# Performance work log

Hardware: AMD Instinct MI355X
Metric: run time of the kernel (lower is better)

The kernel has to match this reference:

```python
import jax, jax.numpy as jnp
import numpy as np

N = 100000   # nodes
E = 600000   # edges
D_IN, D_H, D_OUT = 128, 128, 128


def glorot(key, shape):
    lim = float(np.sqrt(6.0 / (shape[0] + shape[1])))
    return jax.random.uniform(key, shape, jnp.float32, -lim, lim)


def setup_inputs() -> dict:
    key = jax.random.key(0)
    k1, k2, k3, k4 = jax.random.split(key, 4)
    x = jax.random.normal(k1, (N, D_IN), jnp.float32)
    edge_index = jax.random.randint(k2, (2, E), 0, N, jnp.int64)
    W1 = glorot(k3, (D_IN, D_H))
    b1 = jnp.zeros((D_H,), jnp.float32)
    W2 = glorot(k4, (D_H, D_OUT))
    b2 = jnp.zeros((D_OUT,), jnp.float32)
    return {"x": x, "W1": W1, "b1": b1, "W2": W2, "b2": b2, "edge_index": edge_index}


def gcn_conv(x, W, b, src, dst, n):
    # GCNConv: D^{-1/2}(A+I)D^{-1/2} X W + b  (self loops already in src/dst)
    h = x @ W                                   # [N, d_out]
    ones = jnp.ones(src.shape[0], h.dtype)
    deg = jax.ops.segment_sum(ones, dst, num_segments=n)      # in-degree incl self loop
    dinv = jnp.where(deg > 0, jax.lax.rsqrt(deg), 0.0)        # deg^{-1/2}
    norm = dinv[src] * dinv[dst]                              # [E+N]
    msgs = h[src] * norm[:, None]                             # gather + scale
    out = jax.ops.segment_sum(msgs, dst, num_segments=n)      # scatter-add to targets
    return out + b


def reference(x, W1, b1, W2, b2, edge_index):
    loop = jnp.arange(N, dtype=edge_index.dtype)
    src = jnp.concatenate([edge_index[0], loop])
    dst = jnp.concatenate([edge_index[1], loop])
    h = gcn_conv(x, W1, b1, src, dst, N)
    h = jax.nn.relu(h)  # dropout is a no-op in eval mode
    return gcn_conv(h, W2, b2, src, dst, N)
```

## Files before the change

### kernel.cpp

```cpp
#include <hip/hip_runtime.h>

#define NFEAT 128

typedef __attribute__((ext_vector_type(8))) short bf16x8;
typedef __attribute__((ext_vector_type(4))) float f32x4;

__device__ inline ushort f2b(float v) {
  unsigned u = __builtin_bit_cast(unsigned, v);
  return (ushort)((u + 0x7FFFu + ((u >> 16) & 1u)) >> 16);
}


__global__ __launch_bounds__(256) void k_hist(const int* __restrict__ dst,
                                              int* __restrict__ cnt, int E, int N) {
  int range = blockIdx.x & 7, chunk = blockIdx.x >> 3;
  int lo = (int)(((long long)range * N) >> 3);
  int hi = (int)(((long long)(range + 1) * N) >> 3);
  int base = chunk * 1024;
#pragma unroll
  for (int j = 0; j < 4; j++) {
    int i = base + j * 256 + threadIdx.x;
    if (i < E) {
      int d = dst[i];
      if ((unsigned)(d - lo) < (unsigned)(hi - lo)) atomicAdd(&cnt[d], 1);
    }
  }
}

__global__ __launch_bounds__(256) void k_scan_blocks(const int* __restrict__ cnt,
                                                     int* __restrict__ rowptr,
                                                     int* __restrict__ bsum,
                                                     float* __restrict__ dinv, int n) {
  __shared__ int s[256];
  int tid = threadIdx.x;
  int idx = blockIdx.x * 1024 + tid * 4;
  int v[4];
  int sum = 0;
#pragma unroll
  for (int j = 0; j < 4; j++) {
    int c = 0;
    if (idx + j < n) {
      c = cnt[idx + j];
      dinv[idx + j] = rsqrtf((float)(c + 1));
    }
    v[j] = (idx + j < n) ? ((c + 3) & ~3) : 0;
    sum += v[j];
  }
  s[tid] = sum;
  __syncthreads();
  for (int off = 1; off < 256; off <<= 1) {
    int t = (tid >= off) ? s[tid - off] : 0;
    __syncthreads();
    s[tid] += t;
    __syncthreads();
  }
  if (tid == 255) bsum[blockIdx.x] = s[255];
  int run = s[tid] - sum;
#pragma unroll
  for (int j = 0; j < 4; j++) {
    if (idx + j < n) rowptr[idx + j] = run;
    run += v[j];
  }
}

__global__ __launch_bounds__(256) void k_scan_addcur(int* __restrict__ rowptr,
                                                     const int* __restrict__ bsum,
                                                     int* __restrict__ cursor,
                                                     int n, int nb) {
  __shared__ int s[256];
  int tid = threadIdx.x;
  int v = (tid < nb) ? bsum[tid] : 0;
  s[tid] = v;
  __syncthreads();
  for (int off = 1; off < 256; off <<= 1) {
    int t = (tid >= off) ? s[tid - off] : 0;
    __syncthreads();
    s[tid] += t;
    __syncthreads();
  }
  int total = s[255];
  __syncthreads();
  int ex = s[tid] - v;
  __syncthreads();
  s[tid] = ex;
  __syncthreads();
  int i = blockIdx.x * 256 + tid;
  if (i < n) {
    int rp = rowptr[i] + s[i >> 10];
    rowptr[i] = rp;
    cursor[i] = rp;
  }
  if (i == 0) rowptr[n] = total;
}

__global__ __launch_bounds__(256) void k_scatter(const int* __restrict__ src,
                                                 const int* __restrict__ dst,
                                                 const float* __restrict__ dinv,
                                                 int* __restrict__ cursor,
                                                 int2* __restrict__ csr2, int E, int N) {
  int range = blockIdx.x & 7, chunk = blockIdx.x >> 3;
  int lo = (int)(((long long)range * N) >> 3);
  int hi = (int)(((long long)(range + 1) * N) >> 3);
  int base = chunk * 1024;
#pragma unroll
  for (int j = 0; j < 4; j++) {
    int i = base + j * 256 + threadIdx.x;
    if (i < E) {
      int d = dst[i];
      if ((unsigned)(d - lo) < (unsigned)(hi - lo)) {
        int s = src[i];
        int p = atomicAdd(&cursor[d], 1);
        int2 v;
        v.x = s;
        v.y = __float_as_int(dinv[s]);
        csr2[p] = v;
      }
    }
  }
}

__global__ __launch_bounds__(256) void k_cast_w(const float* __restrict__ W1,
                                                const float* __restrict__ W2,
                                                ushort* __restrict__ WT1,
                                                ushort* __restrict__ WT2) {
  int b = blockIdx.x;
  const float* W = (b < 64) ? W1 : W2;
  ushort* WT = (b < 64) ? WT1 : WT2;
  int idx = (b & 63) * 256 + threadIdx.x;
  int k = idx >> 7, nn = idx & 127;
  WT[nn * 128 + k] = f2b(W[idx]);
}


template <bool AFP32>
__global__ __launch_bounds__(256) void k_gemm(const void* __restrict__ Av,
                                              const ushort* __restrict__ WT,
                                              ushort* __restrict__ out, int n) {
  __shared__ ushort sW[128][136];
  int tid = threadIdx.x;
  {
    int r = tid >> 1, hh = tid & 1;
    const uint4* srcp = (const uint4*)(WT + r * 128 + hh * 64);
    uint4* dstp = (uint4*)(&sW[r][hh * 64]);
#pragma unroll
    for (int j = 0; j < 8; j++) dstp[j] = srcp[j];
  }
  __syncthreads();

  int wave = tid >> 6;
  int lane = tid & 63;
  int l16 = lane & 15;
  int quad = lane >> 4;
  int rowBase = blockIdx.x * 128 + wave * 32;

  bf16x8 afrag[2][4];
#pragma unroll
  for (int rt = 0; rt < 2; rt++) {
    int row = rowBase + rt * 16 + l16;
    row = min(row, n - 1);
    if (AFP32) {
      const float* Ap = (const float*)Av + (size_t)row * NFEAT + quad * 8;
#pragma unroll
      for (int ks = 0; ks < 4; ks++) {
        float4 f0 = *(const float4*)(Ap + ks * 32);
        float4 f1 = *(const float4*)(Ap + ks * 32 + 4);
        ushort t[8] = {f2b(f0.x), f2b(f0.y), f2b(f0.z), f2b(f0.w),
                       f2b(f1.x), f2b(f1.y), f2b(f1.z), f2b(f1.w)};
        afrag[rt][ks] = *(const bf16x8*)t;
      }
    } else {
      const ushort* Ap = (const ushort*)Av + (size_t)row * NFEAT + quad * 8;
#pragma unroll
      for (int ks = 0; ks < 4; ks++) afrag[rt][ks] = *(const bf16x8*)(Ap + ks * 32);
    }
  }

#pragma unroll
  for (int ct = 0; ct < 8; ct++) {
    bf16x8 bfrag[4];
#pragma unroll
    for (int ks = 0; ks < 4; ks++)
      bfrag[ks] = *(const bf16x8*)(&sW[ct * 16 + l16][ks * 32 + quad * 8]);
    f32x4 acc[2] = {{0.f, 0.f, 0.f, 0.f}, {0.f, 0.f, 0.f, 0.f}};
#pragma unroll
    for (int rt = 0; rt < 2; rt++)
#pragma unroll
      for (int ks = 0; ks < 4; ks++)
        acc[rt] = __builtin_amdgcn_mfma_f32_16x16x32_bf16(afrag[rt][ks], bfrag[ks],
                                                          acc[rt], 0, 0, 0);
#pragma unroll
    for (int rt = 0; rt < 2; rt++)
#pragma unroll
      for (int r = 0; r < 4; r++) {
        int row = rowBase + rt * 16 + quad * 4 + r;
        if (row < n) out[(size_t)row * NFEAT + ct * 16 + l16] = f2b(acc[rt][r]);
      }
  }
}


__global__ __launch_bounds__(256) void k_agg(const ushort* __restrict__ h,
                                             const float* __restrict__ dinv,
                                             const int* __restrict__ rowptr,
                                             const int2* __restrict__ csr2,
                                             const float* __restrict__ bias,
                                             ushort* __restrict__ out_bf,
                                             float* __restrict__ out_f32,
                                             int n, int relu_bf) {
  int node = blockIdx.x * 8 + (threadIdx.x >> 5);
  if (node >= n) return;
  int c = (threadIdx.x & 31) * 4;
  float di = dinv[node];

  uint2 hv = *(const uint2*)(h + (size_t)node * NFEAT + c);
  float a0 = di * __uint_as_float(hv.x << 16);
  float a1 = di * __uint_as_float(hv.x & 0xffff0000u);
  float a2 = di * __uint_as_float(hv.y << 16);
  float a3 = di * __uint_as_float(hv.y & 0xffff0000u);

  int e = rowptr[node], end = rowptr[node + 1];
  for (; e < end; e += 4) {
    int2 p0 = csr2[e], p1 = csr2[e + 1], p2 = csr2[e + 2], p3 = csr2[e + 3];
    uint2 h0 = *(const uint2*)(h + (size_t)p0.x * NFEAT + c);
    uint2 h1 = *(const uint2*)(h + (size_t)p1.x * NFEAT + c);
    uint2 h2 = *(const uint2*)(h + (size_t)p2.x * NFEAT + c);
    uint2 h3 = *(const uint2*)(h + (size_t)p3.x * NFEAT + c);
    float w0 = __int_as_float(p0.y), w1 = __int_as_float(p1.y);
    float w2 = __int_as_float(p2.y), w3 = __int_as_float(p3.y);
    a0 = fmaf(w0, __uint_as_float(h0.x << 16), a0);
    a1 = fmaf(w0, __uint_as_float(h0.x & 0xffff0000u), a1);
    a2 = fmaf(w0, __uint_as_float(h0.y << 16), a2);
    a3 = fmaf(w0, __uint_as_float(h0.y & 0xffff0000u), a3);
    a0 = fmaf(w1, __uint_as_float(h1.x << 16), a0);
    a1 = fmaf(w1, __uint_as_float(h1.x & 0xffff0000u), a1);
    a2 = fmaf(w1, __uint_as_float(h1.y << 16), a2);
    a3 = fmaf(w1, __uint_as_float(h1.y & 0xffff0000u), a3);
    a0 = fmaf(w2, __uint_as_float(h2.x << 16), a0);
    a1 = fmaf(w2, __uint_as_float(h2.x & 0xffff0000u), a1);
    a2 = fmaf(w2, __uint_as_float(h2.y << 16), a2);
    a3 = fmaf(w2, __uint_as_float(h2.y & 0xffff0000u), a3);
    a0 = fmaf(w3, __uint_as_float(h3.x << 16), a0);
    a1 = fmaf(w3, __uint_as_float(h3.x & 0xffff0000u), a1);
    a2 = fmaf(w3, __uint_as_float(h3.y << 16), a2);
    a3 = fmaf(w3, __uint_as_float(h3.y & 0xffff0000u), a3);
  }

  float4 b = *(const float4*)(bias + c);
  float o0 = fmaf(di, a0, b.x);
  float o1 = fmaf(di, a1, b.y);
  float o2 = fmaf(di, a2, b.z);
  float o3 = fmaf(di, a3, b.w);
  if (relu_bf) {
    o0 = fmaxf(o0, 0.f); o1 = fmaxf(o1, 0.f);
    o2 = fmaxf(o2, 0.f); o3 = fmaxf(o3, 0.f);
    uint2 pk;
    pk.x = f2b(o0) | ((unsigned)f2b(o1) << 16);
    pk.y = f2b(o2) | ((unsigned)f2b(o3) << 16);
    *(uint2*)(out_bf + (size_t)node * NFEAT + c) = pk;
  } else {
    float4 o = {o0, o1, o2, o3};
    *(float4*)(out_f32 + (size_t)node * NFEAT + c) = o;
  }
}


extern "C" void kernel_launch(void* const* d_in, const int* in_sizes, int n_in,
                              void* d_out, int out_size, void* d_ws, size_t ws_size,
                              hipStream_t stream) {
  const float* x = (const float*)d_in[0];
  const float* W1 = (const float*)d_in[1];
  const float* b1 = (const float*)d_in[2];
  const float* W2 = (const float*)d_in[3];
  const float* b2 = (const float*)d_in[4];
  const int* ei = (const int*)d_in[5];

  const int N = in_sizes[0] / NFEAT;
  const int E = in_sizes[5] / 2;
  const int* srcIdx = ei;
  const int* dstIdx = ei + E;

  char* p = (char*)d_ws;
  auto alloc = [&](size_t bytes) {
    char* r = p;
    p += (bytes + 255) & ~(size_t)255;
    return r;
  };
  int* cnt = (int*)alloc((size_t)N * 4);
  int2* csr2 = (int2*)alloc((size_t)(E + 3 * N + 8) * 8);
  char* memset_end = p;
  int* cursor = (int*)alloc((size_t)N * 4);
  float* dinv = (float*)alloc((size_t)N * 4);
  int* rowptr = (int*)alloc((size_t)(N + 1) * 4);
  int* bsum = (int*)alloc(1024);
  ushort* WT1 = (ushort*)alloc(NFEAT * NFEAT * 2);
  ushort* WT2 = (ushort*)alloc(NFEAT * NFEAT * 2);
  ushort* t1 = (ushort*)alloc((size_t)N * NFEAT * 2);
  ushort* h2 = (ushort*)alloc((size_t)N * NFEAT * 2);
  ushort* h1 = (ushort*)d_out;
  float* out = (float*)d_out;

  hipMemsetAsync(cnt, 0, (size_t)(memset_end - (char*)cnt), stream);

  int nb = (N + 1023) / 1024;
  int gEx = ((E + 1023) / 1024) * 8;

  k_hist<<<gEx, 256, 0, stream>>>(dstIdx, cnt, E, N);
  k_scan_blocks<<<nb, 256, 0, stream>>>(cnt, rowptr, bsum, dinv, N);
  k_scan_addcur<<<(N + 255) / 256, 256, 0, stream>>>(rowptr, bsum, cursor, N, nb);
  k_scatter<<<gEx, 256, 0, stream>>>(srcIdx, dstIdx, dinv, cursor, csr2, E, N);
  k_cast_w<<<128, 256, 0, stream>>>(W1, W2, WT1, WT2);

  int gG = (N + 127) / 128;
  int gA = (N + 7) / 8;

  k_gemm<true><<<gG, 256, 0, stream>>>(x, WT1, h1, N);
  k_agg<<<gA, 256, 0, stream>>>(h1, dinv, rowptr, csr2, b1, t1, nullptr, N, 1);
  k_gemm<false><<<gG, 256, 0, stream>>>(t1, WT2, h2, N);
  k_agg<<<gA, 256, 0, stream>>>(h2, dinv, rowptr, csr2, b2, nullptr, out, N, 0);
}
```

Baseline: 262.6 us.

## Fold self-loop into CSR, pad rows to 8, vectorize edge and CSR loads

Puts the self-loop entry into the CSR at build time and pads each row to a multiple of 8. The aggregation loop can then read 8 neighbour entries with four 16-byte loads and unroll over 8 gathers, with no separate self-term load. The histogram and scatter kernels now read edge indices as int4 vectors. Padding grows the CSR buffer and adds wasted zero-weight gathers on low-degree nodes. The change to a per-thread contiguous index pattern also alters how atomics are grouped.

```diff
diff --git a/kernel.cpp b/kernel.cpp
--- a/kernel.cpp
+++ b/kernel.cpp
@@ -16,13 +16,19 @@
   int range = blockIdx.x & 7, chunk = blockIdx.x >> 3;
   int lo = (int)(((long long)range * N) >> 3);
   int hi = (int)(((long long)(range + 1) * N) >> 3);
-  int base = chunk * 1024;
-#pragma unroll
-  for (int j = 0; j < 4; j++) {
-    int i = base + j * 256 + threadIdx.x;
-    if (i < E) {
-      int d = dst[i];
-      if ((unsigned)(d - lo) < (unsigned)(hi - lo)) atomicAdd(&cnt[d], 1);
+  int i = chunk * 1024 + threadIdx.x * 4;
+  if (i + 3 < E) {
+    int4 d4 = *(const int4*)(dst + i);
+    if ((unsigned)(d4.x - lo) < (unsigned)(hi - lo)) atomicAdd(&cnt[d4.x], 1);
+    if ((unsigned)(d4.y - lo) < (unsigned)(hi - lo)) atomicAdd(&cnt[d4.y], 1);
+    if ((unsigned)(d4.z - lo) < (unsigned)(hi - lo)) atomicAdd(&cnt[d4.z], 1);
+    if ((unsigned)(d4.w - lo) < (unsigned)(hi - lo)) atomicAdd(&cnt[d4.w], 1);
+  } else {
+    for (int j = 0; j < 4; j++) {
+      if (i + j < E) {
+        int d = dst[i + j];
+        if ((unsigned)(d - lo) < (unsigned)(hi - lo)) atomicAdd(&cnt[d], 1);
+      }
     }
   }
 }
@@ -43,7 +49,7 @@
       c = cnt[idx + j];
       dinv[idx + j] = rsqrtf((float)(c + 1));
     }
-    v[j] = (idx + j < n) ? ((c + 3) & ~3) : 0;
+    v[j] = (idx + j < n) ? ((c + 8) & ~7) : 0;
     sum += v[j];
   }
   s[tid] = sum;
@@ -66,6 +72,8 @@
 __global__ __launch_bounds__(256) void k_scan_addcur(int* __restrict__ rowptr,
                                                      const int* __restrict__ bsum,
                                                      int* __restrict__ cursor,
+                                                     const float* __restrict__ dinv,
+                                                     int2* __restrict__ csr2,
                                                      int n, int nb) {
   __shared__ int s[256];
   int tid = threadIdx.x;
@@ -88,7 +96,11 @@
   if (i < n) {
     int rp = rowptr[i] + s[i >> 10];
     rowptr[i] = rp;
-    cursor[i] = rp;
+    cursor[i] = rp + 1;
+    int2 self;
+    self.x = i;
+    self.y = __float_as_int(dinv[i]);
+    csr2[rp] = self;
   }
   if (i == 0) rowptr[n] = total;
 }
@@ -101,19 +113,34 @@
   int range = blockIdx.x & 7, chunk = blockIdx.x >> 3;
   int lo = (int)(((long long)range * N) >> 3);
   int hi = (int)(((long long)(range + 1) * N) >> 3);
-  int base = chunk * 1024;
-#pragma unroll
-  for (int j = 0; j < 4; j++) {
-    int i = base + j * 256 + threadIdx.x;
-    if (i < E) {
-      int d = dst[i];
-      if ((unsigned)(d - lo) < (unsigned)(hi - lo)) {
-        int s = src[i];
-        int p = atomicAdd(&cursor[d], 1);
+  int i = chunk * 1024 + threadIdx.x * 4;
+  if (i + 3 < E) {
+    int4 d4 = *(const int4*)(dst + i);
+    int4 s4 = *(const int4*)(src + i);
+    int dd[4] = {d4.x, d4.y, d4.z, d4.w};
+    int ss[4] = {s4.x, s4.y, s4.z, s4.w};
+#pragma unroll
+    for (int j = 0; j < 4; j++) {
+      if ((unsigned)(dd[j] - lo) < (unsigned)(hi - lo)) {
+        int p = atomicAdd(&cursor[dd[j]], 1);
         int2 v;
-        v.x = s;
-        v.y = __float_as_int(dinv[s]);
+        v.x = ss[j];
+        v.y = __float_as_int(dinv[ss[j]]);
         csr2[p] = v;
+      }
+    }
+  } else {
+    for (int j = 0; j < 4; j++) {
+      if (i + j < E) {
+        int d = dst[i + j];
+        if ((unsigned)(d - lo) < (unsigned)(hi - lo)) {
+          int s = src[i + j];
+          int p = atomicAdd(&cursor[d], 1);
+          int2 v;
+          v.x = s;
+          v.y = __float_as_int(dinv[s]);
+          csr2[p] = v;
+        }
       }
     }
   }
@@ -210,23 +237,26 @@
   int node = blockIdx.x * 8 + (threadIdx.x >> 5);
   if (node >= n) return;
   int c = (threadIdx.x & 31) * 4;
-  float di = dinv[node];
-
-  uint2 hv = *(const uint2*)(h + (size_t)node * NFEAT + c);
-  float a0 = di * __uint_as_float(hv.x << 16);
-  float a1 = di * __uint_as_float(hv.x & 0xffff0000u);
-  float a2 = di * __uint_as_float(hv.y << 16);
-  float a3 = di * __uint_as_float(hv.y & 0xffff0000u);
+  float a0 = 0.f, a1 = 0.f, a2 = 0.f, a3 = 0.f;
 
   int e = rowptr[node], end = rowptr[node + 1];
-  for (; e < end; e += 4) {
-    int2 p0 = csr2[e], p1 = csr2[e + 1], p2 = csr2[e + 2], p3 = csr2[e + 3];
-    uint2 h0 = *(const uint2*)(h + (size_t)p0.x * NFEAT + c);
-    uint2 h1 = *(const uint2*)(h + (size_t)p1.x * NFEAT + c);
-    uint2 h2 = *(const uint2*)(h + (size_t)p2.x * NFEAT + c);
-    uint2 h3 = *(const uint2*)(h + (size_t)p3.x * NFEAT + c);
-    float w0 = __int_as_float(p0.y), w1 = __int_as_float(p1.y);
-    float w2 = __int_as_float(p2.y), w3 = __int_as_float(p3.y);
+  for (; e < end; e += 8) {
+    int4 q0 = *(const int4*)(csr2 + e);
+    int4 q1 = *(const int4*)(csr2 + e + 2);
+    int4 q2 = *(const int4*)(csr2 + e + 4);
+    int4 q3 = *(const int4*)(csr2 + e + 6);
+    uint2 h0 = *(const uint2*)(h + (size_t)q0.x * NFEAT + c);
+    uint2 h1 = *(const uint2*)(h + (size_t)q0.z * NFEAT + c);
+    uint2 h2 = *(const uint2*)(h + (size_t)q1.x * NFEAT + c);
+    uint2 h3 = *(const uint2*)(h + (size_t)q1.z * NFEAT + c);
+    uint2 h4 = *(const uint2*)(h + (size_t)q2.x * NFEAT + c);
+    uint2 h5 = *(const uint2*)(h + (size_t)q2.z * NFEAT + c);
+    uint2 h6 = *(const uint2*)(h + (size_t)q3.x * NFEAT + c);
+    uint2 h7 = *(const uint2*)(h + (size_t)q3.z * NFEAT + c);
+    float w0 = __int_as_float(q0.y), w1 = __int_as_float(q0.w);
+    float w2 = __int_as_float(q1.y), w3 = __int_as_float(q1.w);
+    float w4 = __int_as_float(q2.y), w5 = __int_as_float(q2.w);
+    float w6 = __int_as_float(q3.y), w7 = __int_as_float(q3.w);
     a0 = fmaf(w0, __uint_as_float(h0.x << 16), a0);
     a1 = fmaf(w0, __uint_as_float(h0.x & 0xffff0000u), a1);
     a2 = fmaf(w0, __uint_as_float(h0.y << 16), a2);
@@ -243,8 +273,25 @@
     a1 = fmaf(w3, __uint_as_float(h3.x & 0xffff0000u), a1);
     a2 = fmaf(w3, __uint_as_float(h3.y << 16), a2);
     a3 = fmaf(w3, __uint_as_float(h3.y & 0xffff0000u), a3);
-  }
-
+    a0 = fmaf(w4, __uint_as_float(h4.x << 16), a0);
+    a1 = fmaf(w4, __uint_as_float(h4.x & 0xffff0000u), a1);
+    a2 = fmaf(w4, __uint_as_float(h4.y << 16), a2);
+    a3 = fmaf(w4, __uint_as_float(h4.y & 0xffff0000u), a3);
+    a0 = fmaf(w5, __uint_as_float(h5.x << 16), a0);
+    a1 = fmaf(w5, __uint_as_float(h5.x & 0xffff0000u), a1);
+    a2 = fmaf(w5, __uint_as_float(h5.y << 16), a2);
+    a3 = fmaf(w5, __uint_as_float(h5.y & 0xffff0000u), a3);
+    a0 = fmaf(w6, __uint_as_float(h6.x << 16), a0);
+    a1 = fmaf(w6, __uint_as_float(h6.x & 0xffff0000u), a1);
+    a2 = fmaf(w6, __uint_as_float(h6.y << 16), a2);
+    a3 = fmaf(w6, __uint_as_float(h6.y & 0xffff0000u), a3);
+    a0 = fmaf(w7, __uint_as_float(h7.x << 16), a0);
+    a1 = fmaf(w7, __uint_as_float(h7.x & 0xffff0000u), a1);
+    a2 = fmaf(w7, __uint_as_float(h7.y << 16), a2);
+    a3 = fmaf(w7, __uint_as_float(h7.y & 0xffff0000u), a3);
+  }
+
+  float di = dinv[node];
   float4 b = *(const float4*)(bias + c);
   float o0 = fmaf(di, a0, b.x);
   float o1 = fmaf(di, a1, b.y);
@@ -286,7 +333,7 @@
     return r;
   };
   int* cnt = (int*)alloc((size_t)N * 4);
-  int2* csr2 = (int2*)alloc((size_t)(E + 3 * N + 8) * 8);
+  int2* csr2 = (int2*)alloc((size_t)(E + 8 * N + 16) * 8);
   char* memset_end = p;
   int* cursor = (int*)alloc((size_t)N * 4);
   float* dinv = (float*)alloc((size_t)N * 4);
@@ -306,7 +353,8 @@
 
   k_hist<<<gEx, 256, 0, stream>>>(dstIdx, cnt, E, N);
   k_scan_blocks<<<nb, 256, 0, stream>>>(cnt, rowptr, bsum, dinv, N);
-  k_scan_addcur<<<(N + 255) / 256, 256, 0, stream>>>(rowptr, bsum, cursor, N, nb);
+  k_scan_addcur<<<(N + 255) / 256, 256, 0, stream>>>(rowptr, bsum, cursor, dinv, csr2,
+                                                     N, nb);
   k_scatter<<<gEx, 256, 0, stream>>>(srcIdx, dstIdx, dinv, cursor, csr2, E, N);
   k_cast_w<<<128, 256, 0, stream>>>(W1, W2, WT1, WT2);
 
```

Result: no change. 265.9 us (+1.3%).
